# Optimization experiments

Hardware: AMD Instinct MI355X
Metric: run time of the kernel (lower is better)

Reference implementation:

```python
import jax, jax.numpy as jnp
import numpy as np

B, IN, OUT = 131072, 512, 512


def setup_inputs() -> dict:
    key = jax.random.key(0)
    k1, k2 = jax.random.split(key)
    x = jax.random.normal(k1, (B, IN), dtype=jnp.float32)
    # matches reset_parameters: normal(0, sqrt(1/in_features))
    weight = jax.random.normal(k2, (OUT, IN), dtype=jnp.float32) * jnp.sqrt(1.0 / IN)
    bias = jnp.zeros((OUT,), dtype=jnp.float32)
    return {"x": x, "weight": weight, "bias": bias}


def _binarize(w):
    # deterministic sign binarization: w >= 0 -> +1, else -1
    return jnp.where(w >= 0, 1.0, -1.0).astype(w.dtype)


def reference(x, weight, bias):
    wb = _binarize(weight)            # [out, in], values in {-1, +1}
    # out = x @ wb.T + bias           # [B, out]
    return jnp.einsum("bi,oi->bo", x, wb) + bias
```

## Files before the change

### kernel.cpp

```cpp
#include <hip/hip_runtime.h>
#include <stdint.h>


#define BATCH   131072
#define IN_F    512
#define OUT_F   512
#define BM      64
#define NCH     8
#define BUFB    16384

using f32x4  = __attribute__((ext_vector_type(4))) float;
using f32x16 = __attribute__((ext_vector_type(16))) float;
using short8 = __attribute__((ext_vector_type(8))) short;
using usv8   = __attribute__((ext_vector_type(8))) unsigned short;
using u32    = uint32_t;

__global__ void prep_w(const float* __restrict__ W, unsigned short* __restrict__ wf) {
    int t = blockIdx.x * blockDim.x + threadIdx.x;
    int l  = t & 63;
    int nf = (t >> 6) & 15;
    int kt = t >> 10;
    int n = nf * 32 + (l & 31);
    int k = kt * 16 + ((l >> 5) << 3);
    const float* src = W + (size_t)n * IN_F + k;
    f32x4 w0 = *(const f32x4*)(src);
    f32x4 w1 = *(const f32x4*)(src + 4);
    usv8 o;
#pragma unroll
    for (int j = 0; j < 4; ++j) {
        o[j]     = (w0[j] >= 0.0f) ? 0x3F80u : 0xBF80u;
        o[j + 4] = (w1[j] >= 0.0f) ? 0x3F80u : 0xBF80u;
    }
    *(usv8*)(wf + (size_t)t * 8) = o;
}

__global__ __launch_bounds__(512, 2) void gemm_bin(
    const float* __restrict__ X, const unsigned short* __restrict__ WF,
    const float* __restrict__ bias, float* __restrict__ out) {

    __shared__ __align__(16) char smem[4 * BUFB];

    const int tid  = threadIdx.x;
    const int lane = tid & 63;
    const int wv   = tid >> 6;
    const int m0   = blockIdx.x * BM;

    const int dr   = wv * 4 + (lane >> 4);
    const int ds4  = ((lane & 15) ^ (dr & 15)) << 2;
    const float* src0 = X + (size_t)(m0 + dr) * IN_F + ds4;
    const float* src1 = src0 + (size_t)32 * IN_F;

#define ISSUE_DMA(ck_)                                                         \
    {                                                                          \
        char* b_ = smem + ((ck_) & 3) * BUFB + wv * 1024;                      \
        __builtin_amdgcn_global_load_lds(                                      \
            (const __attribute__((address_space(1))) void*)(src0 + (ck_) * 64),\
            (__attribute__((address_space(3))) void*)(b_), 16, 0, 0);          \
        __builtin_amdgcn_global_load_lds(                                      \
            (const __attribute__((address_space(1))) void*)(src1 + (ck_) * 64),\
            (__attribute__((address_space(3))) void*)(b_ + 8192), 16, 0, 0);   \
    }

    const short8* wb = (const short8*)(WF) + ((size_t)(wv * 2) * 64 + lane);
    short8 bf[2][4][2];
#define LDB_ALL(bi_, ck_)                                                      \
    {                                                                          \
        _Pragma("unroll")                                                      \
        for (int g = 0; g < 4; ++g)                                            \
            _Pragma("unroll")                                                  \
            for (int fn = 0; fn < 2; ++fn)                                     \
                bf[bi_][g][fn] = wb[((ck_) * 4 + g) * 1024 + fn * 64];         \
    }

    const int arow = (lane & 31) * 256;
    const int aq32 = (lane >> 5) << 5;
    const int aswz = (lane & 15) << 4;

#define LDA_CVT(dst, ab_, kt4_)                                                \
    {                                                                          \
        _Pragma("unroll")                                                      \
        for (int rg = 0; rg < 2; ++rg) {                                       \
            const char* p_  = (ab_) + rg * 8192 + arow;                        \
            const int  blo_ = (((kt4_) << 6) + aq32) ^ aswz;                   \
            f32x4 lo_ = *(const f32x4*)(p_ + blo_);                            \
            f32x4 hi_ = *(const f32x4*)(p_ + (blo_ ^ 16));                     \
            u32 w0_, w1_, w2_, w3_;                                            \
            asm("v_cvt_pk_bf16_f32 %0, %1, %2" : "=v"(w0_)                     \
                : "v"(lo_[0]), "v"(lo_[1]));                                   \
            asm("v_cvt_pk_bf16_f32 %0, %1, %2" : "=v"(w1_)                     \
                : "v"(lo_[2]), "v"(lo_[3]));                                   \
            asm("v_cvt_pk_bf16_f32 %0, %1, %2" : "=v"(w2_)                     \
                : "v"(hi_[0]), "v"(hi_[1]));                                   \
            asm("v_cvt_pk_bf16_f32 %0, %1, %2" : "=v"(w3_)                     \
                : "v"(hi_[2]), "v"(hi_[3]));                                   \
            union { u32 w[4]; short8 v; } pk_;                                 \
            pk_.w[0] = w0_; pk_.w[1] = w1_; pk_.w[2] = w2_; pk_.w[3] = w3_;    \
            dst[rg] = pk_.v;                                                   \
        }                                                                      \
    }

    f32x16 acc[2][2];
#pragma unroll
    for (int fn = 0; fn < 2; ++fn) {
        const float bv = bias[wv * 64 + fn * 32 + (lane & 31)];
#pragma unroll
        for (int rg = 0; rg < 2; ++rg)
#pragma unroll
            for (int r = 0; r < 16; ++r) acc[rg][fn][r] = bv;
    }
    __builtin_amdgcn_sched_barrier(0);

    ISSUE_DMA(0);
    __builtin_amdgcn_sched_barrier(0);
    LDB_ALL(0, 0);
    __builtin_amdgcn_sched_barrier(0);
    ISSUE_DMA(1);
    __builtin_amdgcn_sched_barrier(0);

#pragma unroll
    for (int ck = 0; ck < NCH; ++ck) {
        if (ck + 1 < NCH) LDB_ALL((ck + 1) & 1, ck + 1);
        __builtin_amdgcn_sched_barrier(0);
        if (ck < NCH - 1) asm volatile("s_waitcnt vmcnt(18)" ::: "memory");
        else              asm volatile("s_waitcnt vmcnt(8)"  ::: "memory");
        __builtin_amdgcn_sched_barrier(0);
        __builtin_amdgcn_s_barrier();
        __builtin_amdgcn_sched_barrier(0);
        if (ck + 2 < NCH) ISSUE_DMA(ck + 2);
        __builtin_amdgcn_sched_barrier(0);

        const char* ab = smem + (ck & 3) * BUFB;
        short8 af[2];
#pragma unroll
        for (int kt4 = 0; kt4 < 4; ++kt4) {
            LDA_CVT(af, ab, kt4);
            __builtin_amdgcn_s_setprio(1);
#pragma unroll
            for (int rg = 0; rg < 2; ++rg)
#pragma unroll
                for (int fn = 0; fn < 2; ++fn)
                    acc[rg][fn] = __builtin_amdgcn_mfma_f32_32x32x16_bf16(
                        af[rg], bf[ck & 1][kt4][fn], acc[rg][fn], 0, 0, 0);
            __builtin_amdgcn_s_setprio(0);
        }
    }
#undef ISSUE_DMA
#undef LDB_ALL
#undef LDA_CVT

    const int c     = lane & 31;
    const int rbase = (lane >> 5) << 2;
#pragma unroll
    for (int rg = 0; rg < 2; ++rg)
#pragma unroll
        for (int fn = 0; fn < 2; ++fn)
#pragma unroll
            for (int r = 0; r < 16; ++r) {
                const int row = rg * 32 + (r & 3) + 8 * (r >> 2) + rbase;
                out[(size_t)(m0 + row) * OUT_F + wv * 64 + fn * 32 + c] =
                    acc[rg][fn][r];
            }
}

extern "C" void kernel_launch(void* const* d_in, const int* in_sizes, int n_in,
                              void* d_out, int out_size, void* d_ws, size_t ws_size,
                              hipStream_t stream) {
    const float* X    = (const float*)d_in[0];
    const float* W    = (const float*)d_in[1];
    const float* bias = (const float*)d_in[2];
    float* o          = (float*)d_out;
    unsigned short* wf = (unsigned short*)d_ws;

    hipLaunchKernelGGL(prep_w, dim3(128), dim3(256), 0, stream, W, wf);
    hipLaunchKernelGGL(gemm_bin, dim3(BATCH / BM), dim3(512), 0, stream,
                       X, wf, bias, o);
}
```

Baseline: 141.8 us.

## Split output columns across two blocks per row strip to raise occupancy

Each 64-row strip is now handled by two blocks, each owning 256 output columns, so the grid doubles and each wave keeps only one 32-column accumulator pair instead of two. Launch bounds go to 4 blocks per CU and block indices are remapped so paired halves share a strip, which should let the second block's X reads hit in L2. The DMA issue is moved ahead of the wait and barrier, and the vmcnt thresholds are retuned to match. In exchange, X is loaded and converted twice, doubling the A-side global traffic and the conversion work, while the working set per block shrinks and more blocks can overlap latency.

```diff
diff --git a/kernel.cpp b/kernel.cpp
--- a/kernel.cpp
+++ b/kernel.cpp
@@ -34,7 +34,7 @@
     *(usv8*)(wf + (size_t)t * 8) = o;
 }
 
-__global__ __launch_bounds__(512, 2) void gemm_bin(
+__global__ __launch_bounds__(512, 4) void gemm_bin(
     const float* __restrict__ X, const unsigned short* __restrict__ WF,
     const float* __restrict__ bias, float* __restrict__ out) {
 
@@ -43,7 +43,12 @@
     const int tid  = threadIdx.x;
     const int lane = tid & 63;
     const int wv   = tid >> 6;
-    const int m0   = blockIdx.x * BM;
+
+    const int d     = blockIdx.x;
+    const int strip = ((d >> 4) << 3) | (d & 7);
+    const int half  = (d >> 3) & 1;
+    const int m0    = strip * BM;
+    const int col0  = half * 256 + wv * 32;
 
     const int dr   = wv * 4 + (lane >> 4);
     const int ds4  = ((lane & 15) ^ (dr & 15)) << 2;
@@ -61,15 +66,13 @@
             (__attribute__((address_space(3))) void*)(b_ + 8192), 16, 0, 0);   \
     }
 
-    const short8* wb = (const short8*)(WF) + ((size_t)(wv * 2) * 64 + lane);
-    short8 bf[2][4][2];
+    const short8* wb = (const short8*)(WF) + ((size_t)(half * 8 + wv) * 64 + lane);
+    short8 bf[2][4];
 #define LDB_ALL(bi_, ck_)                                                      \
     {                                                                          \
         _Pragma("unroll")                                                      \
         for (int g = 0; g < 4; ++g)                                            \
-            _Pragma("unroll")                                                  \
-            for (int fn = 0; fn < 2; ++fn)                                     \
-                bf[bi_][g][fn] = wb[((ck_) * 4 + g) * 1024 + fn * 64];         \
+            bf[bi_][g] = wb[((ck_) * 4 + g) * 1024];                           \
     }
 
     const int arow = (lane & 31) * 256;
@@ -99,15 +102,12 @@
         }                                                                      \
     }
 
-    f32x16 acc[2][2];
+    const float bv = bias[col0 + (lane & 31)];
+    f32x16 acc[2];
 #pragma unroll
-    for (int fn = 0; fn < 2; ++fn) {
-        const float bv = bias[wv * 64 + fn * 32 + (lane & 31)];
+    for (int rg = 0; rg < 2; ++rg)
 #pragma unroll
-        for (int rg = 0; rg < 2; ++rg)
-#pragma unroll
-            for (int r = 0; r < 16; ++r) acc[rg][fn][r] = bv;
-    }
+        for (int r = 0; r < 16; ++r) acc[rg][r] = bv;
     __builtin_amdgcn_sched_barrier(0);
 
     ISSUE_DMA(0);
@@ -121,12 +121,13 @@
     for (int ck = 0; ck < NCH; ++ck) {
         if (ck + 1 < NCH) LDB_ALL((ck + 1) & 1, ck + 1);
         __builtin_amdgcn_sched_barrier(0);
-        if (ck < NCH - 1) asm volatile("s_waitcnt vmcnt(18)" ::: "memory");
-        else              asm volatile("s_waitcnt vmcnt(8)"  ::: "memory");
+        if (ck + 2 < NCH) ISSUE_DMA(ck + 2);
+        __builtin_amdgcn_sched_barrier(0);
+        if (ck < NCH - 2)      asm volatile("s_waitcnt vmcnt(12)" ::: "memory");
+        else if (ck == NCH - 2) asm volatile("s_waitcnt vmcnt(10)" ::: "memory");
+        else                    asm volatile("s_waitcnt vmcnt(4)"  ::: "memory");
         __builtin_amdgcn_sched_barrier(0);
         __builtin_amdgcn_s_barrier();
-        __builtin_amdgcn_sched_barrier(0);
-        if (ck + 2 < NCH) ISSUE_DMA(ck + 2);
         __builtin_amdgcn_sched_barrier(0);
 
         const char* ab = smem + (ck & 3) * BUFB;
@@ -137,10 +138,8 @@
             __builtin_amdgcn_s_setprio(1);
 #pragma unroll
             for (int rg = 0; rg < 2; ++rg)
-#pragma unroll
-                for (int fn = 0; fn < 2; ++fn)
-                    acc[rg][fn] = __builtin_amdgcn_mfma_f32_32x32x16_bf16(
-                        af[rg], bf[ck & 1][kt4][fn], acc[rg][fn], 0, 0, 0);
+                acc[rg] = __builtin_amdgcn_mfma_f32_32x32x16_bf16(
+                    af[rg], bf[ck & 1][kt4], acc[rg], 0, 0, 0);
             __builtin_amdgcn_s_setprio(0);
         }
     }
@@ -153,13 +152,10 @@
 #pragma unroll
     for (int rg = 0; rg < 2; ++rg)
 #pragma unroll
-        for (int fn = 0; fn < 2; ++fn)
-#pragma unroll
-            for (int r = 0; r < 16; ++r) {
-                const int row = rg * 32 + (r & 3) + 8 * (r >> 2) + rbase;
-                out[(size_t)(m0 + row) * OUT_F + wv * 64 + fn * 32 + c] =
-                    acc[rg][fn][r];
-            }
+        for (int r = 0; r < 16; ++r) {
+            const int row = rg * 32 + (r & 3) + 8 * (r >> 2) + rbase;
+            out[(size_t)(m0 + row) * OUT_F + col0 + c] = acc[rg][r];
+        }
 }
 
 extern "C" void kernel_launch(void* const* d_in, const int* in_sizes, int n_in,
@@ -172,6 +168,6 @@
     unsigned short* wf = (unsigned short*)d_ws;
 
     hipLaunchKernelGGL(prep_w, dim3(128), dim3(256), 0, stream, W, wf);
-    hipLaunchKernelGGL(gemm_bin, dim3(BATCH / BM), dim3(512), 0, stream,
+    hipLaunchKernelGGL(gemm_bin, dim3((BATCH / BM) * 2), dim3(512), 0, stream,
                        X, wf, bias, o);
 }
```

Measured after the change: 155.7 us. 1.1x slower.
